# Kernel optimization log

Hardware: AMD Instinct MI355X
Metric: run time of the kernel (lower is better)

The kernel has to match this reference:

```python
import jax, jax.numpy as jnp
import numpy as np

D_MODEL = 1024
N_HEADS = 16
HEAD_DIM = D_MODEL // N_HEADS
B, S = 4, 2048


def setup_inputs() -> dict:
    key = jax.random.key(0)
    ks = jax.random.split(key, 12)
    s = 1.0 / np.sqrt(D_MODEL)
    inp = {
        'query': jax.random.normal(ks[0], (B, S, D_MODEL), jnp.float32),
        'key': jax.random.normal(ks[1], (B, S, D_MODEL), jnp.float32),
        'value': jax.random.normal(ks[2], (B, S, D_MODEL), jnp.float32),
        # causal mask, broadcast over batch and heads: [1,1,S,S]
        'mask': jnp.tril(jnp.ones((S, S), jnp.int32))[None, None],
        'Wq': jax.random.normal(ks[3], (D_MODEL, D_MODEL), jnp.float32) * s,
        'bq': jnp.zeros((D_MODEL,), jnp.float32),
        'Wk': jax.random.normal(ks[4], (D_MODEL, D_MODEL), jnp.float32) * s,
        'bk': jnp.zeros((D_MODEL,), jnp.float32),
        'Wv': jax.random.normal(ks[5], (D_MODEL, D_MODEL), jnp.float32) * s,
        'bv': jnp.zeros((D_MODEL,), jnp.float32),
        'Wo': jax.random.normal(ks[6], (D_MODEL, D_MODEL), jnp.float32) * s,
        'bo': jnp.zeros((D_MODEL,), jnp.float32),
    }
    return inp


def reference(query, key, value, mask, Wq, bq, Wk, bk, Wv, bv, Wo, bo):
    b, q_len, _ = query.shape
    scale = jnp.sqrt(jnp.float32(HEAD_DIM))
    # projections
    q = query @ Wq + bq
    k = key @ Wk + bk
    v = value @ Wv + bv
    # [b, h, s, hd]
    q = q.reshape(b, q_len, N_HEADS, HEAD_DIM).transpose(0, 2, 1, 3)
    k = k.reshape(b, -1, N_HEADS, HEAD_DIM).transpose(0, 2, 1, 3)
    v = v.reshape(b, -1, N_HEADS, HEAD_DIM).transpose(0, 2, 1, 3)
    scores = jnp.einsum('bhqd,bhkd->bhqk', q, k) / scale
    scores = jnp.where(mask == 0, jnp.float32(-jnp.inf), scores)
    attn = jax.nn.softmax(scores, axis=-1)  # dropout p=0 / eval mode
    out = jnp.einsum('bhqk,bhkd->bhqd', attn, v)
    out = out.transpose(0, 2, 1, 3).reshape(b, q_len, D_MODEL)
    return out @ Wo + bo
```

## Files before the change

kernel.cpp:

```cpp
#include <hip/hip_runtime.h>
#include <hip/hip_bf16.h>

typedef __attribute__((ext_vector_type(8))) short short8;
typedef __attribute__((ext_vector_type(4))) float floatx4;
typedef __attribute__((ext_vector_type(4))) unsigned short ushort4v;

#define D_MODEL 1024
#define S_LEN   2048
#define N_HEADS 16
#define HEAD_DIM 64
#define BATCH   4

__device__ __forceinline__ unsigned short f2bf(float x) {
    union { float f; unsigned int u; } v; v.f = x;
    unsigned int u = v.u;
    unsigned int r = (u + 0x7FFFu + ((u >> 16) & 1u)) >> 16;
    return (unsigned short)r;
}
__device__ __forceinline__ unsigned short f2bf_trunc(float x) {
    union { float f; unsigned int u; } v; v.f = x;
    return (unsigned short)(v.u >> 16);
}

__device__ __forceinline__ void gload_lds16(const void* g, void* s) {
    __builtin_amdgcn_global_load_lds(
        (const __attribute__((address_space(1))) void*)g,
        (__attribute__((address_space(3))) void*)s, 16, 0, 0);
}

struct Conv3 {
    const float* src[3];
    unsigned short* dst[3];
};

__global__ __launch_bounds__(256) void conv_bf16(Conv3 a) {
    const float* s = a.src[blockIdx.z];
    unsigned short* d = a.dst[blockIdx.z];
    size_t i = ((size_t)blockIdx.x * 256 + threadIdx.x) * 8;
    float4 f0 = *(const float4*)(s + i);
    float4 f1 = *(const float4*)(s + i + 4);
    short8 v;
    v[0] = (short)f2bf(f0.x); v[1] = (short)f2bf(f0.y);
    v[2] = (short)f2bf(f0.z); v[3] = (short)f2bf(f0.w);
    v[4] = (short)f2bf(f1.x); v[5] = (short)f2bf(f1.y);
    v[6] = (short)f2bf(f1.z); v[7] = (short)f2bf(f1.w);
    *(short8*)(d + i) = v;
}

struct Trans4 {
    const float* W[4];
    unsigned short* Wt[4];
};

__global__ __launch_bounds__(256) void transpose_w(Trans4 args) {
    __shared__ unsigned short tile[32][33];
    const float* W = args.W[blockIdx.z];
    unsigned short* Wt = args.Wt[blockIdx.z];
    int n0 = blockIdx.x * 32;
    int k0 = blockIdx.y * 32;
    int t = threadIdx.x;
    int r = t >> 5, c = t & 31;
    for (int i = 0; i < 4; ++i) {
        int k = k0 + r + i * 8;
        tile[r + i * 8][c] = f2bf(W[(size_t)k * D_MODEL + n0 + c]);
    }
    __syncthreads();
    for (int i = 0; i < 4; ++i) {
        int n = n0 + r + i * 8;
        Wt[(size_t)n * D_MODEL + k0 + c] = tile[c][r + i * 8];
    }
}

struct GemmIn {
    const unsigned short* A;
    const unsigned short* Bt;
    const float* bias;
    void* C;
    int mode;
};
struct Gemm3 { GemmIn g[3]; };

__global__ __launch_bounds__(256) void gemm_tile(Gemm3 args) {
    constexpr int K = D_MODEL, N = D_MODEL;
    GemmIn g = args.g[blockIdx.z];
    __shared__ __align__(16) unsigned short As[128 * 64];
    __shared__ __align__(16) unsigned short Bs[128 * 64];

    int m0 = blockIdx.x * 128;
    int n0 = blockIdx.y * 128;
    int t = threadIdx.x;
    int wave = t >> 6, lane = t & 63;
    int wm = wave >> 1, wn = wave & 1;
    int quad = lane >> 4, l16 = lane & 15;

    int r_base = wave * 16 + (lane >> 2);
    int c_base = (lane & 3) * 8;
    const unsigned short* gA = g.A + (size_t)(m0 + r_base) * K + c_base;
    const unsigned short* gB = g.Bt + (size_t)(n0 + r_base) * K + c_base;
    unsigned short* sA = &As[wave * 512];
    unsigned short* sB = &Bs[wave * 512];

    floatx4 acc[4][4] = {};

    for (int k0 = 0; k0 < K; k0 += 64) {
        for (int c = 0; c < 2; ++c)
            for (int h = 0; h < 2; ++h) {
                size_t goff = (size_t)(h * 64) * K + k0 + c * 32;
                int loff = c * 4096 + h * 2048;
                gload_lds16(gA + goff, sA + loff);
                gload_lds16(gB + goff, sB + loff);
            }
        __syncthreads();

        for (int c = 0; c < 2; ++c) {
            short8 af[4], bfr[4];
            for (int i = 0; i < 4; ++i)
                af[i] = *(const short8*)
                    &As[c * 4096 + (wm * 64 + i * 16 + l16) * 32 + quad * 8];
            for (int j = 0; j < 4; ++j)
                bfr[j] = *(const short8*)
                    &Bs[c * 4096 + (wn * 64 + j * 16 + l16) * 32 + quad * 8];
            for (int i = 0; i < 4; ++i)
                for (int j = 0; j < 4; ++j)
                    acc[i][j] = __builtin_amdgcn_mfma_f32_16x16x32_bf16(
                        af[i], bfr[j], acc[i][j], 0, 0, 0);
        }
        __syncthreads();
    }

    if (g.mode == 2) {
        unsigned short* Ct = (unsigned short*)g.C;
        for (int j = 0; j < 4; ++j) {
            int col = n0 + wn * 64 + j * 16 + l16;
            int h = col >> 6, dd = col & 63;
            float bv = g.bias[col];
            for (int i = 0; i < 4; ++i) {
                int row0 = m0 + wm * 64 + i * 16 + quad * 4;
                int bb = row0 >> 11, s = row0 & 2047;
                ushort4v u;
                for (int r = 0; r < 4; ++r) u[r] = f2bf(acc[i][j][r] + bv);
                *(ushort4v*)(Ct + ((size_t)(bb * 16 + h) * 64 + dd) * 2048 + s) = u;
            }
        }
    } else {
        for (int j = 0; j < 4; ++j) {
            int col = n0 + wn * 64 + j * 16 + l16;
            float bv = g.bias[col];
            for (int i = 0; i < 4; ++i) {
                for (int r = 0; r < 4; ++r) {
                    int row = m0 + wm * 64 + i * 16 + quad * 4 + r;
                    float v = acc[i][j][r] + bv;
                    if (g.mode == 1)
                        ((float*)g.C)[(size_t)row * N + col] = v;
                    else
                        ((unsigned short*)g.C)[(size_t)row * N + col] = f2bf(v);
                }
            }
        }
    }
}

__global__ __launch_bounds__(512) void flash_attn(
    const unsigned short* __restrict__ Qp,
    const unsigned short* __restrict__ Kp,
    const unsigned short* __restrict__ Vtg,
    unsigned short* __restrict__ Op) {
    constexpr int S = S_LEN, D = D_MODEL;
    __shared__ __align__(16) unsigned short Ks[64 * 64];
    __shared__ __align__(16) unsigned short Vs[64 * 64];
    __shared__ __align__(16) unsigned short Ps[8][16][72];

    int pair = blockIdx.x;
    int bh = blockIdx.y;
    int b = bh >> 4;
    int t = threadIdx.x;
    int wave = t >> 6, lane = t & 63;
    int quad = lane >> 4, l16 = lane & 15;

    const size_t head_off = (size_t)b * S * D + (size_t)(bh & 15) * HEAD_DIM;
    const unsigned short* Khead = Kp + head_off;
    const unsigned short* Vhead = Vtg + (size_t)bh * 64 * S;

    int q0l = pair * 128, q0h = (15 - pair) * 128;
    int qgl = q0l + wave * 16 + l16;
    int qgh = q0h + wave * 16 + l16;

    const unsigned short* qpl = Qp + head_off + (size_t)qgl * D + quad * 8;
    short8 ql0 = *(const short8*)qpl, ql1 = *(const short8*)(qpl + 32);
    const unsigned short* qph = Qp + head_off + (size_t)qgh * D + quad * 8;
    short8 qh0 = *(const short8*)qph, qh1 = *(const short8*)(qph + 32);

    floatx4 ol[4] = {}, oh[4] = {};
    float ll = 0.f, lh = 0.f;
    const float cs = 0.125f * 1.44269504088896340736f;

    int sw = wave & 3;
    bool doK = wave < 4;
    int srow = sw * 16 + (lane >> 2);
    int scol = (lane & 3) * 8;
    unsigned short* sdst0 = (doK ? Ks : Vs) + sw * 512;
    unsigned short* sdst1 = sdst0 + 2048;

    int wqminl = q0l + wave * 16, wqmaxl = wqminl + 15;
    int wqminh = q0h + wave * 16, wqmaxh = wqminh + 15;

    auto half_step = [&](int k0, int qg, int wqmin, float& l_i,
                         floatx4* o, short8 qb0, short8 qb1) {
        floatx4 st[4];
        for (int gk = 0; gk < 4; ++gk) {
            short8 ka0 = *(const short8*)&Ks[(gk * 16 + l16) * 32 + quad * 8];
            short8 ka1 = *(const short8*)&Ks[2048 + (gk * 16 + l16) * 32 + quad * 8];
            floatx4 s = {};
            s = __builtin_amdgcn_mfma_f32_16x16x32_bf16(ka0, qb0, s, 0, 0, 0);
            s = __builtin_amdgcn_mfma_f32_16x16x32_bf16(ka1, qb1, s, 0, 0, 0);
            st[gk] = s;
        }

        float sv[16];
        float rs = 0.f;
        if (k0 + 63 < wqmin) {
            for (int i = 0; i < 16; ++i) {
                sv[i] = __builtin_amdgcn_exp2f(st[i >> 2][i & 3] * cs);
                rs += sv[i];
            }
        } else {
            for (int gk = 0; gk < 4; ++gk)
                for (int r = 0; r < 4; ++r) {
                    int key = k0 + gk * 16 + quad * 4 + r;
                    float p = (key <= qg)
                        ? __builtin_amdgcn_exp2f(st[gk][r] * cs) : 0.f;
                    sv[gk * 4 + r] = p;
                    rs += p;
                }
        }
        rs += __shfl_xor(rs, 16);
        rs += __shfl_xor(rs, 32);
        l_i += rs;

        for (int gk = 0; gk < 4; ++gk) {
            ushort4v u;
            for (int r = 0; r < 4; ++r) u[r] = f2bf_trunc(sv[gk * 4 + r]);
            *(ushort4v*)&Ps[wave][l16][gk * 16 + quad * 4] = u;
        }

        short8 pf0 = *(const short8*)&Ps[wave][l16][quad * 8];
        short8 pf1 = *(const short8*)&Ps[wave][l16][32 + quad * 8];
        for (int jd = 0; jd < 4; ++jd) {
            short8 va0 = *(const short8*)&Vs[(jd * 16 + l16) * 32 + quad * 8];
            short8 va1 = *(const short8*)&Vs[2048 + (jd * 16 + l16) * 32 + quad * 8];
            o[jd] = __builtin_amdgcn_mfma_f32_16x16x32_bf16(va0, pf0, o[jd], 0, 0, 0);
            o[jd] = __builtin_amdgcn_mfma_f32_16x16x32_bf16(va1, pf1, o[jd], 0, 0, 0);
        }
    };

    int n_kt = 2 * (15 - pair) + 2;
    for (int kt = 0; kt < n_kt; ++kt) {
        int k0 = kt * 64;
        if (doK) {
            gload_lds16(Khead + (size_t)(k0 + srow) * D + scol, sdst0);
            gload_lds16(Khead + (size_t)(k0 + srow) * D + 32 + scol, sdst1);
        } else {
            gload_lds16(Vhead + (size_t)srow * S + k0 + scol, sdst0);
            gload_lds16(Vhead + (size_t)srow * S + k0 + 32 + scol, sdst1);
        }
        __syncthreads();

        if (k0 <= wqmaxl) half_step(k0, qgl, wqminl, ll, ol, ql0, ql1);
        if (k0 <= wqmaxh) half_step(k0, qgh, wqminh, lh, oh, qh0, qh1);
        __syncthreads();
    }

    {
        float inv = 1.0f / ll;
        unsigned short* op = Op + head_off + (size_t)qgl * D;
        for (int jd = 0; jd < 4; ++jd) {
            ushort4v u;
            for (int r = 0; r < 4; ++r) u[r] = f2bf(ol[jd][r] * inv);
            *(ushort4v*)(op + jd * 16 + quad * 4) = u;
        }
    }
    {
        float inv = 1.0f / lh;
        unsigned short* op = Op + head_off + (size_t)qgh * D;
        for (int jd = 0; jd < 4; ++jd) {
            ushort4v u;
            for (int r = 0; r < 4; ++r) u[r] = f2bf(oh[jd][r] * inv);
            *(ushort4v*)(op + jd * 16 + quad * 4) = u;
        }
    }
}

extern "C" void kernel_launch(void* const* d_in, const int* in_sizes, int n_in,
                              void* d_out, int out_size, void* d_ws,
                              size_t ws_size, hipStream_t stream) {
    const float* query = (const float*)d_in[0];
    const float* key   = (const float*)d_in[1];
    const float* value = (const float*)d_in[2];
    const float* Wq = (const float*)d_in[4];
    const float* bq = (const float*)d_in[5];
    const float* Wk = (const float*)d_in[6];
    const float* bk = (const float*)d_in[7];
    const float* Wv = (const float*)d_in[8];
    const float* bv = (const float*)d_in[9];
    const float* Wo = (const float*)d_in[10];
    const float* bo = (const float*)d_in[11];
    float* out = (float*)d_out;

    char* ws = (char*)d_ws;
    const size_t WT_SZ = (size_t)D_MODEL * D_MODEL * 2;
    const size_t X_SZ = (size_t)BATCH * S_LEN * D_MODEL * 2;
    unsigned short* wtq = (unsigned short*)(ws);
    unsigned short* wtk = (unsigned short*)(ws + WT_SZ);
    unsigned short* wtv = (unsigned short*)(ws + 2 * WT_SZ);
    unsigned short* wto = (unsigned short*)(ws + 3 * WT_SZ);
    unsigned short* Qbf = (unsigned short*)(ws + 4 * WT_SZ);
    unsigned short* Kbf = (unsigned short*)(ws + 4 * WT_SZ + X_SZ);
    unsigned short* Vbf = (unsigned short*)(ws + 4 * WT_SZ + 2 * X_SZ);
    unsigned short* Qp  = (unsigned short*)(ws + 4 * WT_SZ + 3 * X_SZ);
    unsigned short* Kp  = (unsigned short*)(ws + 4 * WT_SZ + 4 * X_SZ);
    unsigned short* Vtg = (unsigned short*)(ws + 4 * WT_SZ + 5 * X_SZ);
    unsigned short* Ao  = Qbf;

    Trans4 ta;
    ta.W[0] = Wq; ta.W[1] = Wk; ta.W[2] = Wv; ta.W[3] = Wo;
    ta.Wt[0] = wtq; ta.Wt[1] = wtk; ta.Wt[2] = wtv; ta.Wt[3] = wto;
    transpose_w<<<dim3(32, 32, 4), 256, 0, stream>>>(ta);

    Conv3 ca;
    ca.src[0] = query; ca.src[1] = key; ca.src[2] = value;
    ca.dst[0] = Qbf;   ca.dst[1] = Kbf; ca.dst[2] = Vbf;
    conv_bf16<<<dim3(4096, 1, 3), 256, 0, stream>>>(ca);

    Gemm3 gq;
    gq.g[0].A = Qbf; gq.g[0].Bt = wtq; gq.g[0].bias = bq; gq.g[0].C = Qp;  gq.g[0].mode = 0;
    gq.g[1].A = Kbf; gq.g[1].Bt = wtk; gq.g[1].bias = bk; gq.g[1].C = Kp;  gq.g[1].mode = 0;
    gq.g[2].A = Vbf; gq.g[2].Bt = wtv; gq.g[2].bias = bv; gq.g[2].C = Vtg; gq.g[2].mode = 2;
    gemm_tile<<<dim3(64, 8, 3), 256, 0, stream>>>(gq);

    flash_attn<<<dim3(8, BATCH * N_HEADS), 512, 0, stream>>>(
        Qp, Kp, Vtg, Ao);

    Gemm3 go;
    go.g[0].A = Ao; go.g[0].Bt = wto; go.g[0].bias = bo; go.g[0].C = out; go.g[0].mode = 1;
    gemm_tile<<<dim3(64, 8, 1), 256, 0, stream>>>(go);
}
```

Measured before the change: 347.3 us.

## Replace projection GEMM with 256x256 double-buffered, swizzled, software-pipelined kernel

Replaces the 128x128 single-buffered projection GEMM with a 256x256-tile kernel using 8 waves and a 128KB double-buffered LDS. It also XOR-swizzles the LDS layout and interleaves global-to-LDS loads with MFMA phases through explicit barriers, vmcnt waits and s_setprio. The aim is more operand reuse per tile and hiding load latency behind matrix math. In exchange the grid shrinks to 384 and 128 blocks, which may underfill the CUs, especially for the output projection, and the large LDS footprint limits occupancy.

```diff
diff --git a/kernel.cpp b/kernel.cpp
--- a/kernel.cpp
+++ b/kernel.cpp
@@ -80,75 +80,185 @@
 };
 struct Gemm3 { GemmIn g[3]; };
 
-__global__ __launch_bounds__(256) void gemm_tile(Gemm3 args) {
+#define BAR()   asm volatile("s_barrier" ::: "memory")
+#define LGKM0() asm volatile("s_waitcnt lgkmcnt(0)" ::: "memory")
+#define VMW4()  asm volatile("s_waitcnt vmcnt(4)" ::: "memory")
+#define VMW0()  asm volatile("s_waitcnt vmcnt(0)" ::: "memory")
+
+#define READ_A(BUF, H)                                                         \
+    _Pragma("unroll") for (int ii = 0; ii < 4; ++ii) {                         \
+        aF[ii][0] = *(const short8*)&lds[(BUF)*32768 + aOff + ((H)*4+ii)*512]; \
+        aF[ii][1] = *(const short8*)&lds[(BUF)*32768 + aOff + ((H)*4+ii)*512 + 4096]; \
+    }
+#define READ_B(BUF, J0, DST)                                                   \
+    _Pragma("unroll") for (int jj = 0; jj < 2; ++jj) {                         \
+        DST[jj][0] = *(const short8*)&lds[(BUF)*32768 + bOff + ((J0)+jj)*512]; \
+        DST[jj][1] = *(const short8*)&lds[(BUF)*32768 + bOff + ((J0)+jj)*512 + 4096]; \
+    }
+#define MFMA_Q(I0, BREG, J0)                                                   \
+    __builtin_amdgcn_s_setprio(1);                                             \
+    _Pragma("unroll") for (int ii = 0; ii < 4; ++ii)                           \
+    _Pragma("unroll") for (int jj = 0; jj < 2; ++jj) {                         \
+        acc[(I0)+ii][(J0)+jj] = __builtin_amdgcn_mfma_f32_16x16x32_bf16(       \
+            aF[ii][0], BREG[jj][0], acc[(I0)+ii][(J0)+jj], 0, 0, 0);           \
+        acc[(I0)+ii][(J0)+jj] = __builtin_amdgcn_mfma_f32_16x16x32_bf16(       \
+            aF[ii][1], BREG[jj][1], acc[(I0)+ii][(J0)+jj], 0, 0, 0);           \
+    }                                                                          \
+    __builtin_amdgcn_s_setprio(0)
+
+__global__ __launch_bounds__(512, 2) void gemm_256(Gemm3 args) {
     constexpr int K = D_MODEL, N = D_MODEL;
+    constexpr int NT = K / 64;
+    constexpr int NI = NT / 2;
     GemmIn g = args.g[blockIdx.z];
-    __shared__ __align__(16) unsigned short As[128 * 64];
-    __shared__ __align__(16) unsigned short Bs[128 * 64];
-
-    int m0 = blockIdx.x * 128;
-    int n0 = blockIdx.y * 128;
-    int t = threadIdx.x;
-    int wave = t >> 6, lane = t & 63;
-    int wm = wave >> 1, wn = wave & 1;
-    int quad = lane >> 4, l16 = lane & 15;
-
-    int r_base = wave * 16 + (lane >> 2);
-    int c_base = (lane & 3) * 8;
-    const unsigned short* gA = g.A + (size_t)(m0 + r_base) * K + c_base;
-    const unsigned short* gB = g.Bt + (size_t)(n0 + r_base) * K + c_base;
-    unsigned short* sA = &As[wave * 512];
-    unsigned short* sB = &Bs[wave * 512];
-
-    floatx4 acc[4][4] = {};
-
-    for (int k0 = 0; k0 < K; k0 += 64) {
-        for (int c = 0; c < 2; ++c)
-            for (int h = 0; h < 2; ++h) {
-                size_t goff = (size_t)(h * 64) * K + k0 + c * 32;
-                int loff = c * 4096 + h * 2048;
-                gload_lds16(gA + goff, sA + loff);
-                gload_lds16(gB + goff, sB + loff);
-            }
-        __syncthreads();
-
-        for (int c = 0; c < 2; ++c) {
-            short8 af[4], bfr[4];
-            for (int i = 0; i < 4; ++i)
-                af[i] = *(const short8*)
-                    &As[c * 4096 + (wm * 64 + i * 16 + l16) * 32 + quad * 8];
-            for (int j = 0; j < 4; ++j)
-                bfr[j] = *(const short8*)
-                    &Bs[c * 4096 + (wn * 64 + j * 16 + l16) * 32 + quad * 8];
-            for (int i = 0; i < 4; ++i)
-                for (int j = 0; j < 4; ++j)
-                    acc[i][j] = __builtin_amdgcn_mfma_f32_16x16x32_bf16(
-                        af[i], bfr[j], acc[i][j], 0, 0, 0);
-        }
-        __syncthreads();
+
+    __shared__ __align__(16) unsigned short lds[65536];
+
+    const int m0 = blockIdx.x * 256;
+    const int n0 = blockIdx.y * 256;
+    const int t = threadIdx.x;
+    const int w = t >> 6, lane = t & 63;
+    const int quad = lane >> 4, l16 = lane & 15;
+    const int wm = w >> 2, wn = w & 3;
+
+    const int srow = w * 16 + (lane >> 2);
+    const int scol = ((lane & 3) * 8) ^ ((lane & 32) ? 16 : 0);
+
+    const int fx = (quad * 8) ^ ((l16 & 8) ? 16 : 0);
+    const int aOff = wm * 8192 + l16 * 32 + fx;
+    const int bOff = 16384 + (wn >> 1) * 8192 + ((wn & 1) * 64 + l16) * 32 + fx;
+
+    floatx4 acc[8][4] = {};
+    short8 aF[4][2], bLo[2][2], bHi[2][2];
+
+    auto stageA = [&](int buf, int h, int kt) {
+        const unsigned short* src =
+            g.A + (size_t)(m0 + h * 128 + srow) * K + kt * 64 + scol;
+        unsigned short* dst = &lds[buf * 32768 + h * 8192 + w * 512];
+        gload_lds16(src, dst);
+        gload_lds16(src + 32, dst + 4096);
+    };
+    auto stageB = [&](int buf, int h, int kt) {
+        const unsigned short* src =
+            g.Bt + (size_t)(n0 + h * 128 + srow) * K + kt * 64 + scol;
+        unsigned short* dst = &lds[buf * 32768 + 16384 + h * 8192 + w * 512];
+        gload_lds16(src, dst);
+        gload_lds16(src + 32, dst + 4096);
+    };
+
+    stageB(0, 0, 0); stageB(0, 1, 0);
+    stageA(0, 0, 0); stageA(0, 1, 0);
+    stageB(1, 0, 1); stageB(1, 1, 1);
+    VMW4();
+    BAR();
+
+    for (int n = 0; n < NI - 1; ++n) {
+        const int t0 = 2 * n;
+        READ_A(0, 0); READ_B(0, 0, bLo);
+        stageA(1, 0, t0 + 1);
+        BAR(); LGKM0();
+        MFMA_Q(0, bLo, 0);
+        BAR();
+        READ_B(0, 2, bHi);
+        stageA(1, 1, t0 + 1);
+        BAR(); LGKM0();
+        MFMA_Q(0, bHi, 2);
+        BAR();
+        READ_A(0, 1);
+        stageB(0, 0, t0 + 2);
+        BAR(); LGKM0();
+        MFMA_Q(4, bHi, 2);
+        BAR();
+        stageB(0, 1, t0 + 2);
+        VMW4();
+        BAR();
+        MFMA_Q(4, bLo, 0);
+        BAR();
+        READ_A(1, 0); READ_B(1, 0, bLo);
+        stageA(0, 0, t0 + 2);
+        BAR(); LGKM0();
+        MFMA_Q(0, bLo, 0);
+        BAR();
+        READ_B(1, 2, bHi);
+        stageA(0, 1, t0 + 2);
+        BAR(); LGKM0();
+        MFMA_Q(0, bHi, 2);
+        BAR();
+        READ_A(1, 1);
+        stageB(1, 0, t0 + 3);
+        BAR(); LGKM0();
+        MFMA_Q(4, bHi, 2);
+        BAR();
+        stageB(1, 1, t0 + 3);
+        VMW4();
+        BAR();
+        MFMA_Q(4, bLo, 0);
+        BAR();
+    }
+
+    {
+        READ_A(0, 0); READ_B(0, 0, bLo);
+        stageA(1, 0, NT - 1);
+        BAR(); LGKM0();
+        MFMA_Q(0, bLo, 0);
+        BAR();
+        READ_B(0, 2, bHi);
+        stageA(1, 1, NT - 1);
+        BAR(); LGKM0();
+        MFMA_Q(0, bHi, 2);
+        BAR();
+        READ_A(0, 1);
+        BAR(); LGKM0();
+        MFMA_Q(4, bHi, 2);
+        BAR();
+        VMW0();
+        BAR();
+        MFMA_Q(4, bLo, 0);
+        BAR();
+        READ_A(1, 0); READ_B(1, 0, bLo);
+        BAR(); LGKM0();
+        MFMA_Q(0, bLo, 0);
+        BAR();
+        READ_B(1, 2, bHi);
+        BAR(); LGKM0();
+        MFMA_Q(0, bHi, 2);
+        BAR();
+        READ_A(1, 1);
+        BAR(); LGKM0();
+        MFMA_Q(4, bHi, 2);
+        BAR();
+        BAR();
+        MFMA_Q(4, bLo, 0);
+        BAR();
     }
 
     if (g.mode == 2) {
         unsigned short* Ct = (unsigned short*)g.C;
+#pragma unroll
         for (int j = 0; j < 4; ++j) {
             int col = n0 + wn * 64 + j * 16 + l16;
             int h = col >> 6, dd = col & 63;
             float bv = g.bias[col];
-            for (int i = 0; i < 4; ++i) {
-                int row0 = m0 + wm * 64 + i * 16 + quad * 4;
+#pragma unroll
+            for (int i = 0; i < 8; ++i) {
+                int row0 = m0 + wm * 128 + i * 16 + quad * 4;
                 int bb = row0 >> 11, s = row0 & 2047;
                 ushort4v u;
+#pragma unroll
                 for (int r = 0; r < 4; ++r) u[r] = f2bf(acc[i][j][r] + bv);
                 *(ushort4v*)(Ct + ((size_t)(bb * 16 + h) * 64 + dd) * 2048 + s) = u;
             }
         }
     } else {
+#pragma unroll
         for (int j = 0; j < 4; ++j) {
             int col = n0 + wn * 64 + j * 16 + l16;
             float bv = g.bias[col];
-            for (int i = 0; i < 4; ++i) {
+#pragma unroll
+            for (int i = 0; i < 8; ++i) {
+#pragma unroll
                 for (int r = 0; r < 4; ++r) {
-                    int row = m0 + wm * 64 + i * 16 + quad * 4 + r;
+                    int row = m0 + wm * 128 + i * 16 + quad * 4 + r;
                     float v = acc[i][j][r] + bv;
                     if (g.mode == 1)
                         ((float*)g.C)[(size_t)row * N + col] = v;
@@ -335,12 +445,12 @@
     gq.g[0].A = Qbf; gq.g[0].Bt = wtq; gq.g[0].bias = bq; gq.g[0].C = Qp;  gq.g[0].mode = 0;
     gq.g[1].A = Kbf; gq.g[1].Bt = wtk; gq.g[1].bias = bk; gq.g[1].C = Kp;  gq.g[1].mode = 0;
     gq.g[2].A = Vbf; gq.g[2].Bt = wtv; gq.g[2].bias = bv; gq.g[2].C = Vtg; gq.g[2].mode = 2;
-    gemm_tile<<<dim3(64, 8, 3), 256, 0, stream>>>(gq);
+    gemm_256<<<dim3(32, 4, 3), 512, 0, stream>>>(gq);
 
     flash_attn<<<dim3(8, BATCH * N_HEADS), 512, 0, stream>>>(
         Qp, Kp, Vtg, Ao);
 
     Gemm3 go;
     go.g[0].A = Ao; go.g[0].Bt = wto; go.g[0].bias = bo; go.g[0].C = out; go.g[0].mode = 1;
-    gemm_tile<<<dim3(64, 8, 1), 256, 0, stream>>>(go);
-}
+    gemm_256<<<dim3(32, 4, 1), 512, 0, stream>>>(go);
+}
```

After: 348.3 us. About the same (+0.3%).
